# Kernel optimization log

Measured on AMD Instinct MI355X. Metric: run time of the kernel, lower is better.

## Reference

```python
import jax, jax.numpy as jnp
import numpy as np


def setup_inputs() -> dict:
    key = jax.random.key(0)
    ks = jax.random.split(key, 7)
    B, S, E = 2, 4096, 512
    return {
        "query": jax.random.normal(ks[0], (B, S, E), jnp.float32),
        "key": jax.random.normal(ks[1], (B, S, E), jnp.float32),
        "value": jax.random.normal(ks[2], (B, S, E), jnp.float32),
        "in_proj_weight": jax.random.normal(ks[3], (3 * E, E), jnp.float32) * 0.02,
        "in_proj_bias": jax.random.normal(ks[4], (3 * E,), jnp.float32) * 0.02,
        "out_proj_weight": jax.random.normal(ks[5], (E, E), jnp.float32) * 0.02,
        "out_proj_bias": jax.random.normal(ks[6], (E,), jnp.float32) * 0.02,
        "window_size": 512,
        "stride": 256,
    }


def reference(query, key, value, in_proj_weight, in_proj_bias,
              out_proj_weight, out_proj_bias, window_size, stride):
    B, S, E = query.shape
    H = 8
    hd = E // H
    scale = 1.0 / np.sqrt(hd).astype(np.float32)

    # Project full sequences once (equivalent to projecting each window slice).
    wq, wk, wv = in_proj_weight[:E], in_proj_weight[E:2 * E], in_proj_weight[2 * E:]
    bq, bk, bv = in_proj_bias[:E], in_proj_bias[E:2 * E], in_proj_bias[2 * E:]
    qp = query @ wq.T + bq   # [B,S,E]
    kp = key @ wk.T + bk
    vp = value @ wv.T + bv

    # Overlapping window gather: [nw, W] token indices.
    starts = np.arange(0, S - window_size + 1, stride)
    idx = starts[:, None] + np.arange(window_size)[None, :]  # [nw, W]
    nw, W = idx.shape

    def heads(x):  # [B,S,E] -> [B,nw,W,H,hd]
        return x[:, idx].reshape(B, nw, W, H, hd)

    qh, kh, vh = heads(qp), heads(kp), heads(vp)

    scores = jnp.einsum('bnqhd,bnkhd->bnhqk', qh, kh) * scale  # [B,nw,H,W,W]
    probs = jax.nn.softmax(scores, axis=-1)
    ctx = jnp.einsum('bnhqk,bnkhd->bnqhd', probs, vh)           # [B,nw,W,H,hd]
    ctx = ctx.reshape(B, nw * W, E)                             # concat over windows
    return ctx @ out_proj_weight.T + out_proj_bias              # [B, nw*W, E]
```

## Files before the change

kernel.cpp:

```cpp
#include <hip/hip_runtime.h>
#include <hip/hip_bf16.h>

typedef __bf16 bf16x8 __attribute__((ext_vector_type(8)));
typedef float f32x4 __attribute__((ext_vector_type(4)));
typedef float f32x16 __attribute__((ext_vector_type(16)));

__device__ __forceinline__ ushort f2bf(float f) {
  union { float f; unsigned u; } x; x.f = f;
  unsigned r = x.u + 0x7fffu + ((x.u >> 16) & 1u);
  return (ushort)(r >> 16);
}

__device__ __forceinline__ void gld_lds16(const void* g, void* l) {
  __builtin_amdgcn_global_load_lds(
      (const __attribute__((address_space(1))) void*)g,
      (__attribute__((address_space(3))) void*)l, 16, 0, 0);
}

#define VMWAIT2 asm volatile("s_waitcnt vmcnt(2)" ::: "memory")
#define VMWAIT4 asm volatile("s_waitcnt vmcnt(4)" ::: "memory")
#define VMWAIT0 asm volatile("s_waitcnt vmcnt(0)" ::: "memory")
#define LGKM0   asm volatile("s_waitcnt lgkmcnt(0)" ::: "memory")
#define SCHEDB  __builtin_amdgcn_sched_barrier(0)
#define RBAR    __builtin_amdgcn_s_barrier()

__global__ __launch_bounds__(256) void k_cvt_w(
    const float* __restrict__ wi, const float* __restrict__ wo,
    ushort* __restrict__ dst) {
  const int NWI = 196608, NWO = 65536;
  const int total = NWI + NWO;
  int i = blockIdx.x * 256 + threadIdx.x;
  int stride = gridDim.x * 256;
  for (; i < total; i += stride) {
    const float* s; int j;
    if (i < NWI) { s = wi; j = i; }
    else         { s = wo; j = i - NWI; }
    float4 val = reinterpret_cast<const float4*>(s)[j];
    ushort4 o;
    o.x = f2bf(val.x); o.y = f2bf(val.y); o.z = f2bf(val.z); o.w = f2bf(val.w);
    reinterpret_cast<ushort4*>(dst)[i] = o;
  }
}

__global__ __launch_bounds__(256) void k_gemm_qkv(
    const float* __restrict__ za0, const float* __restrict__ za1,
    const float* __restrict__ za2,
    const ushort* __restrict__ Btbase,
    const float* __restrict__ biasbase,
    ushort* __restrict__ Cbase, float qs)
{
  int bid0 = blockIdx.x;
  int bid = (bid0 & 7) * 96 + (bid0 >> 3);
  int yy = bid & 3;
  int rest = bid >> 2;
  int xx = rest & 63;
  int z = rest >> 6;

  const float* A32 = (z == 0) ? za0 : (z == 1) ? za1 : za2;
  const ushort* Bt = Btbase + (size_t)262144 * z;
  const float* bias = biasbase + 512 * z;
  float osc = (z == 0) ? qs : 1.0f;

  __shared__ ushort As[2][4096];
  __shared__ ushort Bs[3][4096];

  int tid = threadIdx.x;
  int wv = tid >> 6, ln = tid & 63;
  int l15 = ln & 15, lg = ln >> 4;
  int wm = wv >> 1, wn = wv & 1;
  int m0 = xx * 128, n0 = yy * 128;

  int row_s = tid >> 1, kh = (tid & 1) * 16;
  const float* aP = A32 + (size_t)(m0 + row_s) * 512 + kh;
  int ldsOff = row_s * 32 + kh;

#define STAGE_B(KT, BUF)                                                      \
  {                                                                           \
    _Pragma("unroll")                                                         \
    for (int h2 = 0; h2 < 2; ++h2) {                                          \
      int c = h2 * 256 + wv * 64 + ln;                                        \
      int row = c >> 2, kc = (c & 3) * 8;                                     \
      gld_lds16(Bt + (size_t)(n0 + row) * 512 + (KT) * 32 + kc,               \
                (char*)&Bs[BUF][0] + (h2 * 256 + wv * 64) * 16);              \
    }                                                                         \
  }

#define CVT_WRITE_A(F0, F1, F2, F3, BUF)                                      \
  {                                                                           \
    uint w0, w1, w2, w3, w4, w5, w6, w7;                                      \
    asm("v_cvt_pk_bf16_f32 %0, %1, %2" : "=v"(w0) : "v"(F0.x), "v"(F0.y));    \
    asm("v_cvt_pk_bf16_f32 %0, %1, %2" : "=v"(w1) : "v"(F0.z), "v"(F0.w));    \
    asm("v_cvt_pk_bf16_f32 %0, %1, %2" : "=v"(w2) : "v"(F1.x), "v"(F1.y));    \
    asm("v_cvt_pk_bf16_f32 %0, %1, %2" : "=v"(w3) : "v"(F1.z), "v"(F1.w));    \
    asm("v_cvt_pk_bf16_f32 %0, %1, %2" : "=v"(w4) : "v"(F2.x), "v"(F2.y));    \
    asm("v_cvt_pk_bf16_f32 %0, %1, %2" : "=v"(w5) : "v"(F2.z), "v"(F2.w));    \
    asm("v_cvt_pk_bf16_f32 %0, %1, %2" : "=v"(w6) : "v"(F3.x), "v"(F3.y));    \
    asm("v_cvt_pk_bf16_f32 %0, %1, %2" : "=v"(w7) : "v"(F3.z), "v"(F3.w));    \
    uint4 p0; p0.x = w0; p0.y = w1; p0.z = w2; p0.w = w3;                     \
    uint4 p1; p1.x = w4; p1.y = w5; p1.z = w6; p1.w = w7;                     \
    reinterpret_cast<uint4*>(&As[BUF][ldsOff])[0] = p0;                       \
    reinterpret_cast<uint4*>(&As[BUF][ldsOff + 8])[0] = p1;                   \
  }

  f32x4 acc[4][4] = {};

  STAGE_B(0, 0);
  float4 g0 = reinterpret_cast<const float4*>(aP)[0];
  float4 g1 = reinterpret_cast<const float4*>(aP)[1];
  float4 g2 = reinterpret_cast<const float4*>(aP)[2];
  float4 g3 = reinterpret_cast<const float4*>(aP)[3];
  STAGE_B(1, 1);
  VMWAIT2; SCHEDB;
  CVT_WRITE_A(g0, g1, g2, g3, 0);
  LGKM0; SCHEDB;
  RBAR;

#pragma unroll
  for (int kt = 0; kt < 16; ++kt) {
    const int cur = kt & 1;
    const int bcur = kt % 3;
    float4 f0, f1, f2, f3;
    if (kt < 15) {
      const float* ap = aP + (kt + 1) * 32;
      f0 = reinterpret_cast<const float4*>(ap)[0];
      f1 = reinterpret_cast<const float4*>(ap)[1];
      f2 = reinterpret_cast<const float4*>(ap)[2];
      f3 = reinterpret_cast<const float4*>(ap)[3];
    }
    if (kt < 14) STAGE_B(kt + 2, (kt + 2) % 3);

    bf16x8 af[4], bf4[4];
#pragma unroll
    for (int mf = 0; mf < 4; ++mf)
      af[mf] = *reinterpret_cast<const bf16x8*>(&As[cur][(wm * 64 + mf * 16 + l15) * 32 + lg * 8]);
#pragma unroll
    for (int nf = 0; nf < 4; ++nf)
      bf4[nf] = *reinterpret_cast<const bf16x8*>(&Bs[bcur][(wn * 64 + nf * 16 + l15) * 32 + lg * 8]);
#pragma unroll
    for (int mf = 0; mf < 4; ++mf)
#pragma unroll
      for (int nf = 0; nf < 4; ++nf)
        acc[mf][nf] = __builtin_amdgcn_mfma_f32_16x16x32_bf16(af[mf], bf4[nf], acc[mf][nf], 0, 0, 0);

    if (kt < 15) {
      if (kt < 14) { VMWAIT2; } else { VMWAIT0; }
      SCHEDB;
      CVT_WRITE_A(f0, f1, f2, f3, cur ^ 1);
      LGKM0; SCHEDB;
      RBAR;
    }
  }

#pragma unroll
  for (int mf = 0; mf < 4; ++mf)
#pragma unroll
    for (int nf = 0; nf < 4; ++nf)
#pragma unroll
      for (int r = 0; r < 4; ++r) {
        int rr = m0 + wm * 64 + mf * 16 + lg * 4 + r;
        int cc = n0 + wn * 64 + nf * 16 + l15;
        float v = (acc[mf][nf][r] + bias[cc]) * osc;
        (Cbase + (size_t)4194304 * z)[(size_t)rr * 512 + cc] = f2bf(v);
      }
#undef STAGE_B
#undef CVT_WRITE_A
}

__global__ __launch_bounds__(256) void k_gemm_out(
    const ushort* __restrict__ Ab, const ushort* __restrict__ Bt,
    const float* __restrict__ bias, float* __restrict__ C)
{
  int bid0 = blockIdx.x;
  int bid = (bid0 & 7) * 60 + (bid0 >> 3);
  int yy = bid & 3;
  int xx = bid >> 2;

  __shared__ ushort As[3][4096];
  __shared__ ushort Bs[3][4096];

  int tid = threadIdx.x;
  int wv = tid >> 6, ln = tid & 63;
  int l15 = ln & 15, lg = ln >> 4;
  int wm = wv >> 1, wn = wv & 1;
  int m0 = xx * 128, n0 = yy * 128;

#define STAGE_AB(KT, BUF)                                                     \
  {                                                                           \
    _Pragma("unroll")                                                         \
    for (int h2 = 0; h2 < 2; ++h2) {                                          \
      int c = h2 * 256 + wv * 64 + ln;                                        \
      int row = c >> 2, kc = (c & 3) * 8;                                     \
      gld_lds16(Ab + (size_t)(m0 + row) * 512 + (KT) * 32 + kc,               \
                (char*)&As[BUF][0] + (h2 * 256 + wv * 64) * 16);              \
      gld_lds16(Bt + (size_t)(n0 + row) * 512 + (KT) * 32 + kc,               \
                (char*)&Bs[BUF][0] + (h2 * 256 + wv * 64) * 16);              \
    }                                                                         \
  }

  f32x4 acc[4][4] = {};

  STAGE_AB(0, 0);
  STAGE_AB(1, 1);
  VMWAIT4; SCHEDB;
  RBAR;

#pragma unroll
  for (int kt = 0; kt < 16; ++kt) {
    const int bcur = kt % 3;
    if (kt < 14) STAGE_AB(kt + 2, (kt + 2) % 3);

    bf16x8 af[4], bf4[4];
#pragma unroll
    for (int mf = 0; mf < 4; ++mf)
      af[mf] = *reinterpret_cast<const bf16x8*>(&As[bcur][(wm * 64 + mf * 16 + l15) * 32 + lg * 8]);
#pragma unroll
    for (int nf = 0; nf < 4; ++nf)
      bf4[nf] = *reinterpret_cast<const bf16x8*>(&Bs[bcur][(wn * 64 + nf * 16 + l15) * 32 + lg * 8]);
#pragma unroll
    for (int mf = 0; mf < 4; ++mf)
#pragma unroll
      for (int nf = 0; nf < 4; ++nf)
        acc[mf][nf] = __builtin_amdgcn_mfma_f32_16x16x32_bf16(af[mf], bf4[nf], acc[mf][nf], 0, 0, 0);

    if (kt < 15) {
      if (kt < 14) { VMWAIT4; } else { VMWAIT0; }
      SCHEDB;
      RBAR;
    }
  }

#pragma unroll
  for (int mf = 0; mf < 4; ++mf)
#pragma unroll
    for (int nf = 0; nf < 4; ++nf)
#pragma unroll
      for (int r = 0; r < 4; ++r) {
        int rr = m0 + wm * 64 + mf * 16 + lg * 4 + r;
        int cc = n0 + wn * 64 + nf * 16 + l15;
        C[(size_t)rr * 512 + cc] = acc[mf][nf][r] + bias[cc];
      }
#undef STAGE_AB
}

__global__ __launch_bounds__(256, 2) void k_attn(
    const ushort* __restrict__ qp, const ushort* __restrict__ kp,
    const ushort* __restrict__ vp, ushort* __restrict__ ctx)
{
  const int E = 512, SEQ = 4096;
  int bid0 = blockIdx.x;
  int bid = (bid0 & 7) * 60 + (bid0 >> 3);
  int qh = bid & 1;
  int h = (bid >> 1) & 7;
  int n = (bid >> 4) % 15;
  int b = bid / 240;
  int start = n * 256;

  int tid = threadIdx.x;
  int w = tid >> 6, ln = tid & 63;
  int l31 = ln & 31, hi = ln >> 5;

  size_t base = ((size_t)(b * SEQ + start)) * E + h * 64;
  const ushort* Kw = kp + base;
  const ushort* Vw = vp + base;
  const ushort* Qw = qp + base;

  __shared__ ushort Vt[32768];

  {
    int sk = (tid & 63) * 8;
    int sd = (tid >> 6) * 16;
    const ushort* src = Vw + (size_t)sk * E + sd;
    union { uint4 q[2]; ushort u[16]; } R0, R1, R2, R3, R4, R5, R6, R7;
    R0.q[0] = *(const uint4*)(src + 0 * E); R0.q[1] = *(const uint4*)(src + 0 * E + 8);
    R1.q[0] = *(const uint4*)(src + 1 * E); R1.q[1] = *(const uint4*)(src + 1 * E + 8);
    R2.q[0] = *(const uint4*)(src + 2 * E); R2.q[1] = *(const uint4*)(src + 2 * E + 8);
    R3.q[0] = *(const uint4*)(src + 3 * E); R3.q[1] = *(const uint4*)(src + 3 * E + 8);
    R4.q[0] = *(const uint4*)(src + 4 * E); R4.q[1] = *(const uint4*)(src + 4 * E + 8);
    R5.q[0] = *(const uint4*)(src + 5 * E); R5.q[1] = *(const uint4*)(src + 5 * E + 8);
    R6.q[0] = *(const uint4*)(src + 6 * E); R6.q[1] = *(const uint4*)(src + 6 * E + 8);
    R7.q[0] = *(const uint4*)(src + 7 * E); R7.q[1] = *(const uint4*)(src + 7 * E + 8);
#pragma unroll
    for (int d0 = 0; d0 < 16; ++d0) {
      int d = sd + d0;
      uint4 val;
      val.x = (uint)R0.u[d0] | ((uint)R1.u[d0] << 16);
      val.y = (uint)R2.u[d0] | ((uint)R3.u[d0] << 16);
      val.z = (uint)R4.u[d0] | ((uint)R5.u[d0] << 16);
      val.w = (uint)R6.u[d0] | ((uint)R7.u[d0] << 16);
      int off = d * 1024 + ((sk * 2) ^ ((d & 7) << 4));
      *(uint4*)((char*)Vt + off) = val;
    }
  }
  __syncthreads();

  int q0 = qh * 256 + w * 64;

  bf16x8 qa0, qa1, qa2, qa3, qb0, qb1, qb2, qb3;
  {
    const ushort* qra = Qw + (size_t)(q0 + l31) * E + hi * 8;
    const ushort* qrb = qra + (size_t)32 * E;
    qa0 = *reinterpret_cast<const bf16x8*>(qra + 0);
    qa1 = *reinterpret_cast<const bf16x8*>(qra + 16);
    qa2 = *reinterpret_cast<const bf16x8*>(qra + 32);
    qa3 = *reinterpret_cast<const bf16x8*>(qra + 48);
    qb0 = *reinterpret_cast<const bf16x8*>(qrb + 0);
    qb1 = *reinterpret_cast<const bf16x8*>(qrb + 16);
    qb2 = *reinterpret_cast<const bf16x8*>(qrb + 32);
    qb3 = *reinterpret_cast<const bf16x8*>(qrb + 48);
  }

  f32x16 ca0 = {}, ca1 = {}, cb0_ = {}, cb1_ = {};
  float psa = 0.f, psb = 0.f;
  const char* lb = (const char*)Vt;

#pragma unroll
  for (int kb = 0; kb < 16; ++kb) {
    bf16x8 kf0, kf1, kf2, kf3;
    {
      const ushort* kr = Kw + (size_t)(kb * 32 + l31) * E + hi * 8;
      kf0 = *reinterpret_cast<const bf16x8*>(kr + 0);
      kf1 = *reinterpret_cast<const bf16x8*>(kr + 16);
      kf2 = *reinterpret_cast<const bf16x8*>(kr + 32);
      kf3 = *reinterpret_cast<const bf16x8*>(kr + 48);
    }
    bf16x8 vb00, vb01, vb10, vb11;
    {
      int row = l31, rowh = 32 + l31;
      int cb0 = kb * 64 + hi * 16;
      int cb1 = cb0 + 32;
      int xr0 = (row & 7) << 4;
      vb00 = *reinterpret_cast<const bf16x8*>(lb + row * 1024 + (cb0 ^ xr0));
      vb01 = *reinterpret_cast<const bf16x8*>(lb + rowh * 1024 + (cb0 ^ xr0));
      vb10 = *reinterpret_cast<const bf16x8*>(lb + row * 1024 + (cb1 ^ xr0));
      vb11 = *reinterpret_cast<const bf16x8*>(lb + rowh * 1024 + (cb1 ^ xr0));
    }

    f32x16 s1 = {}, s2 = {};
    __builtin_amdgcn_s_setprio(1);
    s1 = __builtin_amdgcn_mfma_f32_32x32x16_bf16(kf0, qa0, s1, 0, 0, 0);
    s2 = __builtin_amdgcn_mfma_f32_32x32x16_bf16(kf0, qb0, s2, 0, 0, 0);
    s1 = __builtin_amdgcn_mfma_f32_32x32x16_bf16(kf1, qa1, s1, 0, 0, 0);
    s2 = __builtin_amdgcn_mfma_f32_32x32x16_bf16(kf1, qb1, s2, 0, 0, 0);
    s1 = __builtin_amdgcn_mfma_f32_32x32x16_bf16(kf2, qa2, s1, 0, 0, 0);
    s2 = __builtin_amdgcn_mfma_f32_32x32x16_bf16(kf2, qb2, s2, 0, 0, 0);
    s1 = __builtin_amdgcn_mfma_f32_32x32x16_bf16(kf3, qa3, s1, 0, 0, 0);
    s2 = __builtin_amdgcn_mfma_f32_32x32x16_bf16(kf3, qb3, s2, 0, 0, 0);
    __builtin_amdgcn_s_setprio(0);

#pragma unroll
    for (int r = 0; r < 16; ++r) s1[r] = __builtin_amdgcn_exp2f(s1[r]);
#pragma unroll
    for (int r = 0; r < 16; ++r) s2[r] = __builtin_amdgcn_exp2f(s2[r]);
    {
      float t0 = (s1[0] + s1[1]) + (s1[2] + s1[3]);
      float t1 = (s1[4] + s1[5]) + (s1[6] + s1[7]);
      float t2 = (s1[8] + s1[9]) + (s1[10] + s1[11]);
      float t3 = (s1[12] + s1[13]) + (s1[14] + s1[15]);
      psa += (t0 + t1) + (t2 + t3);
      float u0 = (s2[0] + s2[1]) + (s2[2] + s2[3]);
      float u1 = (s2[4] + s2[5]) + (s2[6] + s2[7]);
      float u2 = (s2[8] + s2[9]) + (s2[10] + s2[11]);
      float u3 = (s2[12] + s2[13]) + (s2[14] + s2[15]);
      psb += (u0 + u1) + (u2 + u3);
    }

    uint a0, a1, a2, a3, a4, a5, a6, a7;
    asm("v_cvt_pk_bf16_f32 %0, %1, %2" : "=v"(a0) : "v"(s1[0]),  "v"(s1[1]));
    asm("v_cvt_pk_bf16_f32 %0, %1, %2" : "=v"(a1) : "v"(s1[2]),  "v"(s1[3]));
    asm("v_cvt_pk_bf16_f32 %0, %1, %2" : "=v"(a2) : "v"(s1[4]),  "v"(s1[5]));
    asm("v_cvt_pk_bf16_f32 %0, %1, %2" : "=v"(a3) : "v"(s1[6]),  "v"(s1[7]));
    asm("v_cvt_pk_bf16_f32 %0, %1, %2" : "=v"(a4) : "v"(s1[8]),  "v"(s1[9]));
    asm("v_cvt_pk_bf16_f32 %0, %1, %2" : "=v"(a5) : "v"(s1[10]), "v"(s1[11]));
    asm("v_cvt_pk_bf16_f32 %0, %1, %2" : "=v"(a6) : "v"(s1[12]), "v"(s1[13]));
    asm("v_cvt_pk_bf16_f32 %0, %1, %2" : "=v"(a7) : "v"(s1[14]), "v"(s1[15]));
    asm("v_permlane32_swap_b32 %0, %1" : "+v"(a0), "+v"(a2));
    asm("v_permlane32_swap_b32 %0, %1" : "+v"(a1), "+v"(a3));
    asm("v_permlane32_swap_b32 %0, %1" : "+v"(a4), "+v"(a6));
    asm("v_permlane32_swap_b32 %0, %1" : "+v"(a5), "+v"(a7));
    uint b0, b1, b2, b3, b4, b5, b6, b7;
    asm("v_cvt_pk_bf16_f32 %0, %1, %2" : "=v"(b0) : "v"(s2[0]),  "v"(s2[1]));
    asm("v_cvt_pk_bf16_f32 %0, %1, %2" : "=v"(b1) : "v"(s2[2]),  "v"(s2[3]));
    asm("v_cvt_pk_bf16_f32 %0, %1, %2" : "=v"(b2) : "v"(s2[4]),  "v"(s2[5]));
    asm("v_cvt_pk_bf16_f32 %0, %1, %2" : "=v"(b3) : "v"(s2[6]),  "v"(s2[7]));
    asm("v_cvt_pk_bf16_f32 %0, %1, %2" : "=v"(b4) : "v"(s2[8]),  "v"(s2[9]));
    asm("v_cvt_pk_bf16_f32 %0, %1, %2" : "=v"(b5) : "v"(s2[10]), "v"(s2[11]));
    asm("v_cvt_pk_bf16_f32 %0, %1, %2" : "=v"(b6) : "v"(s2[12]), "v"(s2[13]));
    asm("v_cvt_pk_bf16_f32 %0, %1, %2" : "=v"(b7) : "v"(s2[14]), "v"(s2[15]));
    asm("v_permlane32_swap_b32 %0, %1" : "+v"(b0), "+v"(b2));
    asm("v_permlane32_swap_b32 %0, %1" : "+v"(b1), "+v"(b3));
    asm("v_permlane32_swap_b32 %0, %1" : "+v"(b4), "+v"(b6));
    asm("v_permlane32_swap_b32 %0, %1" : "+v"(b5), "+v"(b7));
    union { uint u[4]; bf16x8 v; } A1, A2, B1, B2;
    A1.u[0] = a0; A1.u[1] = a1; A1.u[2] = a2; A1.u[3] = a3;
    A2.u[0] = a4; A2.u[1] = a5; A2.u[2] = a6; A2.u[3] = a7;
    B1.u[0] = b0; B1.u[1] = b1; B1.u[2] = b2; B1.u[3] = b3;
    B2.u[0] = b4; B2.u[1] = b5; B2.u[2] = b6; B2.u[3] = b7;

    __builtin_amdgcn_s_setprio(1);
    ca0  = __builtin_amdgcn_mfma_f32_32x32x16_bf16(A1.v, vb00, ca0, 0, 0, 0);
    cb0_ = __builtin_amdgcn_mfma_f32_32x32x16_bf16(B1.v, vb00, cb0_, 0, 0, 0);
    ca1  = __builtin_amdgcn_mfma_f32_32x32x16_bf16(A1.v, vb01, ca1, 0, 0, 0);
    cb1_ = __builtin_amdgcn_mfma_f32_32x32x16_bf16(B1.v, vb01, cb1_, 0, 0, 0);
    ca0  = __builtin_amdgcn_mfma_f32_32x32x16_bf16(A2.v, vb10, ca0, 0, 0, 0);
    cb0_ = __builtin_amdgcn_mfma_f32_32x32x16_bf16(B2.v, vb10, cb0_, 0, 0, 0);
    ca1  = __builtin_amdgcn_mfma_f32_32x32x16_bf16(A2.v, vb11, ca1, 0, 0, 0);
    cb1_ = __builtin_amdgcn_mfma_f32_32x32x16_bf16(B2.v, vb11, cb1_, 0, 0, 0);
    __builtin_amdgcn_s_setprio(0);
  }

  psa += __shfl_xor(psa, 32);
  psb += __shfl_xor(psb, 32);
  float ria = 1.0f / psa;
  float rib = 1.0f / psb;
  size_t orow0 = (size_t)b * 7680 + (size_t)n * 512 + q0;
#pragma unroll
  for (int r = 0; r < 16; ++r) {
    int qrel = (r & 3) + 8 * (r >> 2) + 4 * hi;
    float r1 = __shfl(ria, qrel);
    float r2 = __shfl(rib, qrel);
    ushort* dA = ctx + (orow0 + qrel) * E + h * 64 + l31;
    ushort* dB = ctx + (orow0 + 32 + qrel) * E + h * 64 + l31;
    dA[0]  = f2bf(ca0[r] * r1);
    dA[32] = f2bf(ca1[r] * r1);
    dB[0]  = f2bf(cb0_[r] * r2);
    dB[32] = f2bf(cb1_[r] * r2);
  }
}

extern "C" void kernel_launch(void* const* d_in, const int* in_sizes, int n_in,
                              void* d_out, int out_size, void* d_ws, size_t ws_size,
                              hipStream_t stream) {
  const float* query = (const float*)d_in[0];
  const float* key   = (const float*)d_in[1];
  const float* value = (const float*)d_in[2];
  const float* ipw   = (const float*)d_in[3];
  const float* ipb   = (const float*)d_in[4];
  const float* opw   = (const float*)d_in[5];
  const float* opb   = (const float*)d_in[6];

  ushort* wib = (ushort*)d_ws;
  ushort* wob = wib + 786432;
  ushort* qp  = wob + 262144;
  ushort* kp  = qp  + 4194304;
  ushort* vp  = kp  + 4194304;
  ushort* ctx = vp  + 4194304;

  const float SC = 0.125f * 1.44269504088896340736f;

  k_cvt_w<<<512, 256, 0, stream>>>(ipw, opw, wib);

  k_gemm_qkv<<<768, 256, 0, stream>>>(
      query, key, value, wib, ipb, qp, SC);

  k_attn<<<480, 256, 0, stream>>>(qp, kp, vp, ctx);

  k_gemm_out<<<480, 256, 0, stream>>>(
      ctx, wob, opb, (float*)d_out);
}
```

Before: 81.72 us.

## Pre-convert Q/K/V activations to bf16 and use async LDS loads in QKV GEMM

Extends the weight conversion kernel so it also converts the query, key and value inputs to bf16 in a workspace buffer. The QKV projection GEMM then reads bf16 A operands through direct global-to-LDS loads with triple buffering, like the output GEMM. The old in-kernel fp32 load, convert and LDS write path is removed. This simplifies the GEMM main loop, but adds a full extra pass that reads the fp32 activations and writes bf16 copies to memory.

```diff
diff --git a/kernel.cpp b/kernel.cpp
--- a/kernel.cpp
+++ b/kernel.cpp
@@ -17,24 +17,27 @@
       (__attribute__((address_space(3))) void*)l, 16, 0, 0);
 }
 
-#define VMWAIT2 asm volatile("s_waitcnt vmcnt(2)" ::: "memory")
-#define VMWAIT4 asm volatile("s_waitcnt vmcnt(4)" ::: "memory")
-#define VMWAIT0 asm volatile("s_waitcnt vmcnt(0)" ::: "memory")
-#define LGKM0   asm volatile("s_waitcnt lgkmcnt(0)" ::: "memory")
-#define SCHEDB  __builtin_amdgcn_sched_barrier(0)
-#define RBAR    __builtin_amdgcn_s_barrier()
-
-__global__ __launch_bounds__(256) void k_cvt_w(
-    const float* __restrict__ wi, const float* __restrict__ wo,
-    ushort* __restrict__ dst) {
+#define VMW4   asm volatile("s_waitcnt vmcnt(4)" ::: "memory")
+#define VMW0   asm volatile("s_waitcnt vmcnt(0)" ::: "memory")
+#define SCHEDB __builtin_amdgcn_sched_barrier(0)
+#define RBAR   __builtin_amdgcn_s_barrier()
+
+__global__ __launch_bounds__(256) void k_cvt_all(
+    const float* __restrict__ q, const float* __restrict__ k,
+    const float* __restrict__ v, const float* __restrict__ wi,
+    const float* __restrict__ wo, ushort* __restrict__ dst) {
+  const int NQ = 1048576;
   const int NWI = 196608, NWO = 65536;
-  const int total = NWI + NWO;
+  const int total = 3 * NQ + NWI + NWO;
   int i = blockIdx.x * 256 + threadIdx.x;
   int stride = gridDim.x * 256;
   for (; i < total; i += stride) {
     const float* s; int j;
-    if (i < NWI) { s = wi; j = i; }
-    else         { s = wo; j = i - NWI; }
+    if (i < NQ)              { s = q;  j = i; }
+    else if (i < 2 * NQ)     { s = k;  j = i - NQ; }
+    else if (i < 3 * NQ)     { s = v;  j = i - 2 * NQ; }
+    else if (i < 3 * NQ + NWI) { s = wi; j = i - 3 * NQ; }
+    else                     { s = wo; j = i - 3 * NQ - NWI; }
     float4 val = reinterpret_cast<const float4*>(s)[j];
     ushort4 o;
     o.x = f2bf(val.x); o.y = f2bf(val.y); o.z = f2bf(val.z); o.w = f2bf(val.w);
@@ -43,8 +46,7 @@
 }
 
 __global__ __launch_bounds__(256) void k_gemm_qkv(
-    const float* __restrict__ za0, const float* __restrict__ za1,
-    const float* __restrict__ za2,
+    const ushort* __restrict__ Abase,
     const ushort* __restrict__ Btbase,
     const float* __restrict__ biasbase,
     ushort* __restrict__ Cbase, float qs)
@@ -56,124 +58,10 @@
   int xx = rest & 63;
   int z = rest >> 6;
 
-  const float* A32 = (z == 0) ? za0 : (z == 1) ? za1 : za2;
+  const ushort* Ab = Abase + (size_t)4194304 * z;
   const ushort* Bt = Btbase + (size_t)262144 * z;
   const float* bias = biasbase + 512 * z;
   float osc = (z == 0) ? qs : 1.0f;
-
-  __shared__ ushort As[2][4096];
-  __shared__ ushort Bs[3][4096];
-
-  int tid = threadIdx.x;
-  int wv = tid >> 6, ln = tid & 63;
-  int l15 = ln & 15, lg = ln >> 4;
-  int wm = wv >> 1, wn = wv & 1;
-  int m0 = xx * 128, n0 = yy * 128;
-
-  int row_s = tid >> 1, kh = (tid & 1) * 16;
-  const float* aP = A32 + (size_t)(m0 + row_s) * 512 + kh;
-  int ldsOff = row_s * 32 + kh;
-
-#define STAGE_B(KT, BUF)                                                      \
-  {                                                                           \
-    _Pragma("unroll")                                                         \
-    for (int h2 = 0; h2 < 2; ++h2) {                                          \
-      int c = h2 * 256 + wv * 64 + ln;                                        \
-      int row = c >> 2, kc = (c & 3) * 8;                                     \
-      gld_lds16(Bt + (size_t)(n0 + row) * 512 + (KT) * 32 + kc,               \
-                (char*)&Bs[BUF][0] + (h2 * 256 + wv * 64) * 16);              \
-    }                                                                         \
-  }
-
-#define CVT_WRITE_A(F0, F1, F2, F3, BUF)                                      \
-  {                                                                           \
-    uint w0, w1, w2, w3, w4, w5, w6, w7;                                      \
-    asm("v_cvt_pk_bf16_f32 %0, %1, %2" : "=v"(w0) : "v"(F0.x), "v"(F0.y));    \
-    asm("v_cvt_pk_bf16_f32 %0, %1, %2" : "=v"(w1) : "v"(F0.z), "v"(F0.w));    \
-    asm("v_cvt_pk_bf16_f32 %0, %1, %2" : "=v"(w2) : "v"(F1.x), "v"(F1.y));    \
-    asm("v_cvt_pk_bf16_f32 %0, %1, %2" : "=v"(w3) : "v"(F1.z), "v"(F1.w));    \
-    asm("v_cvt_pk_bf16_f32 %0, %1, %2" : "=v"(w4) : "v"(F2.x), "v"(F2.y));    \
-    asm("v_cvt_pk_bf16_f32 %0, %1, %2" : "=v"(w5) : "v"(F2.z), "v"(F2.w));    \
-    asm("v_cvt_pk_bf16_f32 %0, %1, %2" : "=v"(w6) : "v"(F3.x), "v"(F3.y));    \
-    asm("v_cvt_pk_bf16_f32 %0, %1, %2" : "=v"(w7) : "v"(F3.z), "v"(F3.w));    \
-    uint4 p0; p0.x = w0; p0.y = w1; p0.z = w2; p0.w = w3;                     \
-    uint4 p1; p1.x = w4; p1.y = w5; p1.z = w6; p1.w = w7;                     \
-    reinterpret_cast<uint4*>(&As[BUF][ldsOff])[0] = p0;                       \
-    reinterpret_cast<uint4*>(&As[BUF][ldsOff + 8])[0] = p1;                   \
-  }
-
-  f32x4 acc[4][4] = {};
-
-  STAGE_B(0, 0);
-  float4 g0 = reinterpret_cast<const float4*>(aP)[0];
-  float4 g1 = reinterpret_cast<const float4*>(aP)[1];
-  float4 g2 = reinterpret_cast<const float4*>(aP)[2];
-  float4 g3 = reinterpret_cast<const float4*>(aP)[3];
-  STAGE_B(1, 1);
-  VMWAIT2; SCHEDB;
-  CVT_WRITE_A(g0, g1, g2, g3, 0);
-  LGKM0; SCHEDB;
-  RBAR;
-
-#pragma unroll
-  for (int kt = 0; kt < 16; ++kt) {
-    const int cur = kt & 1;
-    const int bcur = kt % 3;
-    float4 f0, f1, f2, f3;
-    if (kt < 15) {
-      const float* ap = aP + (kt + 1) * 32;
-      f0 = reinterpret_cast<const float4*>(ap)[0];
-      f1 = reinterpret_cast<const float4*>(ap)[1];
-      f2 = reinterpret_cast<const float4*>(ap)[2];
-      f3 = reinterpret_cast<const float4*>(ap)[3];
-    }
-    if (kt < 14) STAGE_B(kt + 2, (kt + 2) % 3);
-
-    bf16x8 af[4], bf4[4];
-#pragma unroll
-    for (int mf = 0; mf < 4; ++mf)
-      af[mf] = *reinterpret_cast<const bf16x8*>(&As[cur][(wm * 64 + mf * 16 + l15) * 32 + lg * 8]);
-#pragma unroll
-    for (int nf = 0; nf < 4; ++nf)
-      bf4[nf] = *reinterpret_cast<const bf16x8*>(&Bs[bcur][(wn * 64 + nf * 16 + l15) * 32 + lg * 8]);
-#pragma unroll
-    for (int mf = 0; mf < 4; ++mf)
-#pragma unroll
-      for (int nf = 0; nf < 4; ++nf)
-        acc[mf][nf] = __builtin_amdgcn_mfma_f32_16x16x32_bf16(af[mf], bf4[nf], acc[mf][nf], 0, 0, 0);
-
-    if (kt < 15) {
-      if (kt < 14) { VMWAIT2; } else { VMWAIT0; }
-      SCHEDB;
-      CVT_WRITE_A(f0, f1, f2, f3, cur ^ 1);
-      LGKM0; SCHEDB;
-      RBAR;
-    }
-  }
-
-#pragma unroll
-  for (int mf = 0; mf < 4; ++mf)
-#pragma unroll
-    for (int nf = 0; nf < 4; ++nf)
-#pragma unroll
-      for (int r = 0; r < 4; ++r) {
-        int rr = m0 + wm * 64 + mf * 16 + lg * 4 + r;
-        int cc = n0 + wn * 64 + nf * 16 + l15;
-        float v = (acc[mf][nf][r] + bias[cc]) * osc;
-        (Cbase + (size_t)4194304 * z)[(size_t)rr * 512 + cc] = f2bf(v);
-      }
-#undef STAGE_B
-#undef CVT_WRITE_A
-}
-
-__global__ __launch_bounds__(256) void k_gemm_out(
-    const ushort* __restrict__ Ab, const ushort* __restrict__ Bt,
-    const float* __restrict__ bias, float* __restrict__ C)
-{
-  int bid0 = blockIdx.x;
-  int bid = (bid0 & 7) * 60 + (bid0 >> 3);
-  int yy = bid & 3;
-  int xx = bid >> 2;
 
   __shared__ ushort As[3][4096];
   __shared__ ushort Bs[3][4096];
@@ -201,7 +89,7 @@
 
   STAGE_AB(0, 0);
   STAGE_AB(1, 1);
-  VMWAIT4; SCHEDB;
+  VMW4; SCHEDB;
   RBAR;
 
 #pragma unroll
@@ -223,7 +111,84 @@
         acc[mf][nf] = __builtin_amdgcn_mfma_f32_16x16x32_bf16(af[mf], bf4[nf], acc[mf][nf], 0, 0, 0);
 
     if (kt < 15) {
-      if (kt < 14) { VMWAIT4; } else { VMWAIT0; }
+      if (kt < 14) { VMW4; } else { VMW0; }
+      SCHEDB;
+      RBAR;
+    }
+  }
+
+#pragma unroll
+  for (int mf = 0; mf < 4; ++mf)
+#pragma unroll
+    for (int nf = 0; nf < 4; ++nf)
+#pragma unroll
+      for (int r = 0; r < 4; ++r) {
+        int rr = m0 + wm * 64 + mf * 16 + lg * 4 + r;
+        int cc = n0 + wn * 64 + nf * 16 + l15;
+        float v = (acc[mf][nf][r] + bias[cc]) * osc;
+        (Cbase + (size_t)4194304 * z)[(size_t)rr * 512 + cc] = f2bf(v);
+      }
+#undef STAGE_AB
+}
+
+__global__ __launch_bounds__(256) void k_gemm_out(
+    const ushort* __restrict__ Ab, const ushort* __restrict__ Bt,
+    const float* __restrict__ bias, float* __restrict__ C)
+{
+  int bid0 = blockIdx.x;
+  int bid = (bid0 & 7) * 60 + (bid0 >> 3);
+  int yy = bid & 3;
+  int xx = bid >> 2;
+
+  __shared__ ushort As[3][4096];
+  __shared__ ushort Bs[3][4096];
+
+  int tid = threadIdx.x;
+  int wv = tid >> 6, ln = tid & 63;
+  int l15 = ln & 15, lg = ln >> 4;
+  int wm = wv >> 1, wn = wv & 1;
+  int m0 = xx * 128, n0 = yy * 128;
+
+#define STAGE_AB(KT, BUF)                                                     \
+  {                                                                           \
+    _Pragma("unroll")                                                         \
+    for (int h2 = 0; h2 < 2; ++h2) {                                          \
+      int c = h2 * 256 + wv * 64 + ln;                                        \
+      int row = c >> 2, kc = (c & 3) * 8;                                     \
+      gld_lds16(Ab + (size_t)(m0 + row) * 512 + (KT) * 32 + kc,               \
+                (char*)&As[BUF][0] + (h2 * 256 + wv * 64) * 16);              \
+      gld_lds16(Bt + (size_t)(n0 + row) * 512 + (KT) * 32 + kc,               \
+                (char*)&Bs[BUF][0] + (h2 * 256 + wv * 64) * 16);              \
+    }                                                                         \
+  }
+
+  f32x4 acc[4][4] = {};
+
+  STAGE_AB(0, 0);
+  STAGE_AB(1, 1);
+  VMW4; SCHEDB;
+  RBAR;
+
+#pragma unroll
+  for (int kt = 0; kt < 16; ++kt) {
+    const int bcur = kt % 3;
+    if (kt < 14) STAGE_AB(kt + 2, (kt + 2) % 3);
+
+    bf16x8 af[4], bf4[4];
+#pragma unroll
+    for (int mf = 0; mf < 4; ++mf)
+      af[mf] = *reinterpret_cast<const bf16x8*>(&As[bcur][(wm * 64 + mf * 16 + l15) * 32 + lg * 8]);
+#pragma unroll
+    for (int nf = 0; nf < 4; ++nf)
+      bf4[nf] = *reinterpret_cast<const bf16x8*>(&Bs[bcur][(wn * 64 + nf * 16 + l15) * 32 + lg * 8]);
+#pragma unroll
+    for (int mf = 0; mf < 4; ++mf)
+#pragma unroll
+      for (int nf = 0; nf < 4; ++nf)
+        acc[mf][nf] = __builtin_amdgcn_mfma_f32_16x16x32_bf16(af[mf], bf4[nf], acc[mf][nf], 0, 0, 0);
+
+    if (kt < 15) {
+      if (kt < 14) { VMW4; } else { VMW0; }
       SCHEDB;
       RBAR;
     }
@@ -438,7 +403,10 @@
   const float* opw   = (const float*)d_in[5];
   const float* opb   = (const float*)d_in[6];
 
-  ushort* wib = (ushort*)d_ws;
+  ushort* qb  = (ushort*)d_ws;
+  ushort* kb  = qb  + 4194304;
+  ushort* vb  = kb  + 4194304;
+  ushort* wib = vb  + 4194304;
   ushort* wob = wib + 786432;
   ushort* qp  = wob + 262144;
   ushort* kp  = qp  + 4194304;
@@ -447,13 +415,11 @@
 
   const float SC = 0.125f * 1.44269504088896340736f;
 
-  k_cvt_w<<<512, 256, 0, stream>>>(ipw, opw, wib);
-
-  k_gemm_qkv<<<768, 256, 0, stream>>>(
-      query, key, value, wib, ipb, qp, SC);
+  k_cvt_all<<<2048, 256, 0, stream>>>(query, key, value, ipw, opw, qb);
+
+  k_gemm_qkv<<<768, 256, 0, stream>>>(qb, wib, ipb, qp, SC);
 
   k_attn<<<480, 256, 0, stream>>>(qp, kp, vp, ctx);
 
-  k_gemm_out<<<480, 256, 0, stream>>>(
-      ctx, wob, opb, (float*)d_out);
-}
+  k_gemm_out<<<480, 256, 0, stream>>>(ctx, wob, opb, (float*)d_out);
+}
```

Measured after the change: 84.08 us. +2.9%, slower.

## Split attention blocks over head-dim halves to double grid and occupancy

Applied to the files above, without the earlier changes.

Each attention block now handles only half of the 64-wide head dimension for the PV product, which doubles the grid from 480 to 960 blocks. This halves the V-transpose LDS buffer and the output accumulators, and raises the launch-bounds occupancy hint from 2 to 3. The cost is that QK^T scores and softmax are now computed twice per query tile, once for each half. Several macros are renamed with no behavioural change.

```diff
diff --git a/kernel.cpp b/kernel.cpp
--- a/kernel.cpp
+++ b/kernel.cpp
@@ -17,12 +17,12 @@
       (__attribute__((address_space(3))) void*)l, 16, 0, 0);
 }
 
-#define VMWAIT2 asm volatile("s_waitcnt vmcnt(2)" ::: "memory")
-#define VMWAIT4 asm volatile("s_waitcnt vmcnt(4)" ::: "memory")
-#define VMWAIT0 asm volatile("s_waitcnt vmcnt(0)" ::: "memory")
-#define LGKM0   asm volatile("s_waitcnt lgkmcnt(0)" ::: "memory")
-#define SCHEDB  __builtin_amdgcn_sched_barrier(0)
-#define RBAR    __builtin_amdgcn_s_barrier()
+#define VMW2   asm volatile("s_waitcnt vmcnt(2)" ::: "memory")
+#define VMW4   asm volatile("s_waitcnt vmcnt(4)" ::: "memory")
+#define VMW0   asm volatile("s_waitcnt vmcnt(0)" ::: "memory")
+#define LGKM0  asm volatile("s_waitcnt lgkmcnt(0)" ::: "memory")
+#define SCHEDB __builtin_amdgcn_sched_barrier(0)
+#define RBAR   __builtin_amdgcn_s_barrier()
 
 __global__ __launch_bounds__(256) void k_cvt_w(
     const float* __restrict__ wi, const float* __restrict__ wo,
@@ -110,7 +110,7 @@
   float4 g2 = reinterpret_cast<const float4*>(aP)[2];
   float4 g3 = reinterpret_cast<const float4*>(aP)[3];
   STAGE_B(1, 1);
-  VMWAIT2; SCHEDB;
+  VMW2; SCHEDB;
   CVT_WRITE_A(g0, g1, g2, g3, 0);
   LGKM0; SCHEDB;
   RBAR;
@@ -143,7 +143,7 @@
         acc[mf][nf] = __builtin_amdgcn_mfma_f32_16x16x32_bf16(af[mf], bf4[nf], acc[mf][nf], 0, 0, 0);
 
     if (kt < 15) {
-      if (kt < 14) { VMWAIT2; } else { VMWAIT0; }
+      if (kt < 14) { VMW2; } else { VMW0; }
       SCHEDB;
       CVT_WRITE_A(f0, f1, f2, f3, cur ^ 1);
       LGKM0; SCHEDB;
@@ -201,7 +201,7 @@
 
   STAGE_AB(0, 0);
   STAGE_AB(1, 1);
-  VMWAIT4; SCHEDB;
+  VMW4; SCHEDB;
   RBAR;
 
 #pragma unroll
@@ -223,7 +223,7 @@
         acc[mf][nf] = __builtin_amdgcn_mfma_f32_16x16x32_bf16(af[mf], bf4[nf], acc[mf][nf], 0, 0, 0);
 
     if (kt < 15) {
-      if (kt < 14) { VMWAIT4; } else { VMWAIT0; }
+      if (kt < 14) { VMW4; } else { VMW0; }
       SCHEDB;
       RBAR;
     }
@@ -242,17 +242,18 @@
 #undef STAGE_AB
 }
 
-__global__ __launch_bounds__(256, 2) void k_attn(
+__global__ __launch_bounds__(256, 3) void k_attn(
     const ushort* __restrict__ qp, const ushort* __restrict__ kp,
     const ushort* __restrict__ vp, ushort* __restrict__ ctx)
 {
   const int E = 512, SEQ = 4096;
   int bid0 = blockIdx.x;
-  int bid = (bid0 & 7) * 60 + (bid0 >> 3);
-  int qh = bid & 1;
-  int h = (bid >> 1) & 7;
-  int n = (bid >> 4) % 15;
-  int b = bid / 240;
+  int bid = (bid0 & 7) * 120 + (bid0 >> 3);
+  int dh = bid & 1;
+  int qh = (bid >> 1) & 1;
+  int h = (bid >> 2) & 7;
+  int n = (bid >> 5) % 15;
+  int b = bid / 480;
   int start = n * 256;
 
   int tid = threadIdx.x;
@@ -264,23 +265,23 @@
   const ushort* Vw = vp + base;
   const ushort* Qw = qp + base;
 
-  __shared__ ushort Vt[32768];
+  __shared__ ushort Vt[16384];
 
   {
     int sk = (tid & 63) * 8;
-    int sd = (tid >> 6) * 16;
-    const ushort* src = Vw + (size_t)sk * E + sd;
-    union { uint4 q[2]; ushort u[16]; } R0, R1, R2, R3, R4, R5, R6, R7;
-    R0.q[0] = *(const uint4*)(src + 0 * E); R0.q[1] = *(const uint4*)(src + 0 * E + 8);
-    R1.q[0] = *(const uint4*)(src + 1 * E); R1.q[1] = *(const uint4*)(src + 1 * E + 8);
-    R2.q[0] = *(const uint4*)(src + 2 * E); R2.q[1] = *(const uint4*)(src + 2 * E + 8);
-    R3.q[0] = *(const uint4*)(src + 3 * E); R3.q[1] = *(const uint4*)(src + 3 * E + 8);
-    R4.q[0] = *(const uint4*)(src + 4 * E); R4.q[1] = *(const uint4*)(src + 4 * E + 8);
-    R5.q[0] = *(const uint4*)(src + 5 * E); R5.q[1] = *(const uint4*)(src + 5 * E + 8);
-    R6.q[0] = *(const uint4*)(src + 6 * E); R6.q[1] = *(const uint4*)(src + 6 * E + 8);
-    R7.q[0] = *(const uint4*)(src + 7 * E); R7.q[1] = *(const uint4*)(src + 7 * E + 8);
-#pragma unroll
-    for (int d0 = 0; d0 < 16; ++d0) {
+    int sd = (tid >> 6) * 8;
+    const ushort* src = Vw + (size_t)sk * E + dh * 32 + sd;
+    union { uint4 q; ushort u[8]; } R0, R1, R2, R3, R4, R5, R6, R7;
+    R0.q = *(const uint4*)(src + 0 * E);
+    R1.q = *(const uint4*)(src + 1 * E);
+    R2.q = *(const uint4*)(src + 2 * E);
+    R3.q = *(const uint4*)(src + 3 * E);
+    R4.q = *(const uint4*)(src + 4 * E);
+    R5.q = *(const uint4*)(src + 5 * E);
+    R6.q = *(const uint4*)(src + 6 * E);
+    R7.q = *(const uint4*)(src + 7 * E);
+#pragma unroll
+    for (int d0 = 0; d0 < 8; ++d0) {
       int d = sd + d0;
       uint4 val;
       val.x = (uint)R0.u[d0] | ((uint)R1.u[d0] << 16);
@@ -309,7 +310,7 @@
     qb3 = *reinterpret_cast<const bf16x8*>(qrb + 48);
   }
 
-  f32x16 ca0 = {}, ca1 = {}, cb0_ = {}, cb1_ = {};
+  f32x16 ca = {}, cb = {};
   float psa = 0.f, psb = 0.f;
   const char* lb = (const char*)Vt;
 
@@ -323,16 +324,13 @@
       kf2 = *reinterpret_cast<const bf16x8*>(kr + 32);
       kf3 = *reinterpret_cast<const bf16x8*>(kr + 48);
     }
-    bf16x8 vb00, vb01, vb10, vb11;
+    bf16x8 vb0, vb1;
     {
-      int row = l31, rowh = 32 + l31;
       int cb0 = kb * 64 + hi * 16;
       int cb1 = cb0 + 32;
-      int xr0 = (row & 7) << 4;
-      vb00 = *reinterpret_cast<const bf16x8*>(lb + row * 1024 + (cb0 ^ xr0));
-      vb01 = *reinterpret_cast<const bf16x8*>(lb + rowh * 1024 + (cb0 ^ xr0));
-      vb10 = *reinterpret_cast<const bf16x8*>(lb + row * 1024 + (cb1 ^ xr0));
-      vb11 = *reinterpret_cast<const bf16x8*>(lb + rowh * 1024 + (cb1 ^ xr0));
+      int xr0 = (l31 & 7) << 4;
+      vb0 = *reinterpret_cast<const bf16x8*>(lb + l31 * 1024 + (cb0 ^ xr0));
+      vb1 = *reinterpret_cast<const bf16x8*>(lb + l31 * 1024 + (cb1 ^ xr0));
     }
 
     f32x16 s1 = {}, s2 = {};
@@ -397,14 +395,10 @@
     B2.u[0] = b4; B2.u[1] = b5; B2.u[2] = b6; B2.u[3] = b7;
 
     __builtin_amdgcn_s_setprio(1);
-    ca0  = __builtin_amdgcn_mfma_f32_32x32x16_bf16(A1.v, vb00, ca0, 0, 0, 0);
-    cb0_ = __builtin_amdgcn_mfma_f32_32x32x16_bf16(B1.v, vb00, cb0_, 0, 0, 0);
-    ca1  = __builtin_amdgcn_mfma_f32_32x32x16_bf16(A1.v, vb01, ca1, 0, 0, 0);
-    cb1_ = __builtin_amdgcn_mfma_f32_32x32x16_bf16(B1.v, vb01, cb1_, 0, 0, 0);
-    ca0  = __builtin_amdgcn_mfma_f32_32x32x16_bf16(A2.v, vb10, ca0, 0, 0, 0);
-    cb0_ = __builtin_amdgcn_mfma_f32_32x32x16_bf16(B2.v, vb10, cb0_, 0, 0, 0);
-    ca1  = __builtin_amdgcn_mfma_f32_32x32x16_bf16(A2.v, vb11, ca1, 0, 0, 0);
-    cb1_ = __builtin_amdgcn_mfma_f32_32x32x16_bf16(B2.v, vb11, cb1_, 0, 0, 0);
+    ca = __builtin_amdgcn_mfma_f32_32x32x16_bf16(A1.v, vb0, ca, 0, 0, 0);
+    cb = __builtin_amdgcn_mfma_f32_32x32x16_bf16(B1.v, vb0, cb, 0, 0, 0);
+    ca = __builtin_amdgcn_mfma_f32_32x32x16_bf16(A2.v, vb1, ca, 0, 0, 0);
+    cb = __builtin_amdgcn_mfma_f32_32x32x16_bf16(B2.v, vb1, cb, 0, 0, 0);
     __builtin_amdgcn_s_setprio(0);
   }
 
@@ -418,12 +412,8 @@
     int qrel = (r & 3) + 8 * (r >> 2) + 4 * hi;
     float r1 = __shfl(ria, qrel);
     float r2 = __shfl(rib, qrel);
-    ushort* dA = ctx + (orow0 + qrel) * E + h * 64 + l31;
-    ushort* dB = ctx + (orow0 + 32 + qrel) * E + h * 64 + l31;
-    dA[0]  = f2bf(ca0[r] * r1);
-    dA[32] = f2bf(ca1[r] * r1);
-    dB[0]  = f2bf(cb0_[r] * r2);
-    dB[32] = f2bf(cb1_[r] * r2);
+    ctx[(orow0 + qrel) * E + h * 64 + dh * 32 + l31]      = f2bf(ca[r] * r1);
+    ctx[(orow0 + 32 + qrel) * E + h * 64 + dh * 32 + l31] = f2bf(cb[r] * r2);
   }
 }
 
@@ -452,7 +442,7 @@
   k_gemm_qkv<<<768, 256, 0, stream>>>(
       query, key, value, wib, ipb, qp, SC);
 
-  k_attn<<<480, 256, 0, stream>>>(qp, kp, vp, ctx);
+  k_attn<<<960, 256, 0, stream>>>(qp, kp, vp, ctx);
 
   k_gemm_out<<<480, 256, 0, stream>>>(
       ctx, wob, opb, (float*)d_out);
```

New measurement: 96.19 us. +17.7%, slower.

## Stage K tiles through triple-buffered LDS with async global-to-LDS loads in attention

Applied to the files above, without the earlier changes.

The attention kernel used to read each K block straight from global memory into registers inside the loop, which left it exposed to load latency. K tiles now go into a three-slot LDS ring buffer through global_load_lds, prefetched two blocks ahead. Reads use an XOR swizzle to avoid bank conflicts, and vmcnt waits plus a workgroup barrier follow each iteration. This hides K load latency but adds a barrier per iteration and 12KB more LDS, which may lower occupancy.

```diff
diff --git a/kernel.cpp b/kernel.cpp
--- a/kernel.cpp
+++ b/kernel.cpp
@@ -17,12 +17,13 @@
       (__attribute__((address_space(3))) void*)l, 16, 0, 0);
 }
 
-#define VMWAIT2 asm volatile("s_waitcnt vmcnt(2)" ::: "memory")
-#define VMWAIT4 asm volatile("s_waitcnt vmcnt(4)" ::: "memory")
-#define VMWAIT0 asm volatile("s_waitcnt vmcnt(0)" ::: "memory")
-#define LGKM0   asm volatile("s_waitcnt lgkmcnt(0)" ::: "memory")
-#define SCHEDB  __builtin_amdgcn_sched_barrier(0)
-#define RBAR    __builtin_amdgcn_s_barrier()
+#define VMW1   asm volatile("s_waitcnt vmcnt(1)" ::: "memory")
+#define VMW2   asm volatile("s_waitcnt vmcnt(2)" ::: "memory")
+#define VMW4   asm volatile("s_waitcnt vmcnt(4)" ::: "memory")
+#define VMW0   asm volatile("s_waitcnt vmcnt(0)" ::: "memory")
+#define LGKM0  asm volatile("s_waitcnt lgkmcnt(0)" ::: "memory")
+#define SCHEDB __builtin_amdgcn_sched_barrier(0)
+#define RBAR   __builtin_amdgcn_s_barrier()
 
 __global__ __launch_bounds__(256) void k_cvt_w(
     const float* __restrict__ wi, const float* __restrict__ wo,
@@ -110,7 +111,7 @@
   float4 g2 = reinterpret_cast<const float4*>(aP)[2];
   float4 g3 = reinterpret_cast<const float4*>(aP)[3];
   STAGE_B(1, 1);
-  VMWAIT2; SCHEDB;
+  VMW2; SCHEDB;
   CVT_WRITE_A(g0, g1, g2, g3, 0);
   LGKM0; SCHEDB;
   RBAR;
@@ -143,7 +144,7 @@
         acc[mf][nf] = __builtin_amdgcn_mfma_f32_16x16x32_bf16(af[mf], bf4[nf], acc[mf][nf], 0, 0, 0);
 
     if (kt < 15) {
-      if (kt < 14) { VMWAIT2; } else { VMWAIT0; }
+      if (kt < 14) { VMW2; } else { VMW0; }
       SCHEDB;
       CVT_WRITE_A(f0, f1, f2, f3, cur ^ 1);
       LGKM0; SCHEDB;
@@ -201,7 +202,7 @@
 
   STAGE_AB(0, 0);
   STAGE_AB(1, 1);
-  VMWAIT4; SCHEDB;
+  VMW4; SCHEDB;
   RBAR;
 
 #pragma unroll
@@ -223,7 +224,7 @@
         acc[mf][nf] = __builtin_amdgcn_mfma_f32_16x16x32_bf16(af[mf], bf4[nf], acc[mf][nf], 0, 0, 0);
 
     if (kt < 15) {
-      if (kt < 14) { VMWAIT4; } else { VMWAIT0; }
+      if (kt < 14) { VMW4; } else { VMW0; }
       SCHEDB;
       RBAR;
     }
@@ -265,6 +266,7 @@
   const ushort* Qw = qp + base;
 
   __shared__ ushort Vt[32768];
+  __shared__ ushort Ks[3][2048];
 
   {
     int sk = (tid & 63) * 8;
@@ -309,30 +311,47 @@
     qb3 = *reinterpret_cast<const bf16x8*>(qrb + 48);
   }
 
+#define STAGE_K(KB, BUF)                                                      \
+  {                                                                           \
+    int row_ = tid >> 3;                                                      \
+    int cs_ = (tid & 7) * 16;                                                 \
+    int del_ = (cs_ ^ ((row_ & 7) << 4)) >> 1;                                \
+    gld_lds16(Kw + (size_t)((KB) * 32 + row_) * E + del_,                     \
+              (char*)&Ks[BUF][0] + tid * 16);                                 \
+  }
+
   f32x16 ca0 = {}, ca1 = {}, cb0_ = {}, cb1_ = {};
   float psa = 0.f, psb = 0.f;
   const char* lb = (const char*)Vt;
 
+  STAGE_K(0, 0);
+  STAGE_K(1, 1);
+  VMW1; SCHEDB;
+  RBAR;
+
 #pragma unroll
   for (int kb = 0; kb < 16; ++kb) {
+    if (kb < 14) STAGE_K(kb + 2, (kb + 2) % 3);
+
     bf16x8 kf0, kf1, kf2, kf3;
     {
-      const ushort* kr = Kw + (size_t)(kb * 32 + l31) * E + hi * 8;
-      kf0 = *reinterpret_cast<const bf16x8*>(kr + 0);
-      kf1 = *reinterpret_cast<const bf16x8*>(kr + 16);
-      kf2 = *reinterpret_cast<const bf16x8*>(kr + 32);
-      kf3 = *reinterpret_cast<const bf16x8*>(kr + 48);
-    }
-    bf16x8 vb00, vb01, vb10, vb11;
+      const char* kbase = (const char*)&Ks[kb % 3][0] + l31 * 128;
+      int xr = (l31 & 7) << 4;
+      kf0 = *reinterpret_cast<const bf16x8*>(kbase + ((0 * 32 + hi * 16) ^ xr));
+      kf1 = *reinterpret_cast<const bf16x8*>(kbase + ((1 * 32 + hi * 16) ^ xr));
+      kf2 = *reinterpret_cast<const bf16x8*>(kbase + ((2 * 32 + hi * 16) ^ xr));
+      kf3 = *reinterpret_cast<const bf16x8*>(kbase + ((3 * 32 + hi * 16) ^ xr));
+    }
+    bf16x8 vb0, vb1, vb2, vb3;
     {
       int row = l31, rowh = 32 + l31;
       int cb0 = kb * 64 + hi * 16;
       int cb1 = cb0 + 32;
       int xr0 = (row & 7) << 4;
-      vb00 = *reinterpret_cast<const bf16x8*>(lb + row * 1024 + (cb0 ^ xr0));
-      vb01 = *reinterpret_cast<const bf16x8*>(lb + rowh * 1024 + (cb0 ^ xr0));
-      vb10 = *reinterpret_cast<const bf16x8*>(lb + row * 1024 + (cb1 ^ xr0));
-      vb11 = *reinterpret_cast<const bf16x8*>(lb + rowh * 1024 + (cb1 ^ xr0));
+      vb0 = *reinterpret_cast<const bf16x8*>(lb + row * 1024 + (cb0 ^ xr0));
+      vb1 = *reinterpret_cast<const bf16x8*>(lb + rowh * 1024 + (cb0 ^ xr0));
+      vb2 = *reinterpret_cast<const bf16x8*>(lb + row * 1024 + (cb1 ^ xr0));
+      vb3 = *reinterpret_cast<const bf16x8*>(lb + rowh * 1024 + (cb1 ^ xr0));
     }
 
     f32x16 s1 = {}, s2 = {};
@@ -397,16 +416,23 @@
     B2.u[0] = b4; B2.u[1] = b5; B2.u[2] = b6; B2.u[3] = b7;
 
     __builtin_amdgcn_s_setprio(1);
-    ca0  = __builtin_amdgcn_mfma_f32_32x32x16_bf16(A1.v, vb00, ca0, 0, 0, 0);
-    cb0_ = __builtin_amdgcn_mfma_f32_32x32x16_bf16(B1.v, vb00, cb0_, 0, 0, 0);
-    ca1  = __builtin_amdgcn_mfma_f32_32x32x16_bf16(A1.v, vb01, ca1, 0, 0, 0);
-    cb1_ = __builtin_amdgcn_mfma_f32_32x32x16_bf16(B1.v, vb01, cb1_, 0, 0, 0);
-    ca0  = __builtin_amdgcn_mfma_f32_32x32x16_bf16(A2.v, vb10, ca0, 0, 0, 0);
-    cb0_ = __builtin_amdgcn_mfma_f32_32x32x16_bf16(B2.v, vb10, cb0_, 0, 0, 0);
-    ca1  = __builtin_amdgcn_mfma_f32_32x32x16_bf16(A2.v, vb11, ca1, 0, 0, 0);
-    cb1_ = __builtin_amdgcn_mfma_f32_32x32x16_bf16(B2.v, vb11, cb1_, 0, 0, 0);
+    ca0  = __builtin_amdgcn_mfma_f32_32x32x16_bf16(A1.v, vb0, ca0, 0, 0, 0);
+    cb0_ = __builtin_amdgcn_mfma_f32_32x32x16_bf16(B1.v, vb0, cb0_, 0, 0, 0);
+    ca1  = __builtin_amdgcn_mfma_f32_32x32x16_bf16(A1.v, vb1, ca1, 0, 0, 0);
+    cb1_ = __builtin_amdgcn_mfma_f32_32x32x16_bf16(B1.v, vb1, cb1_, 0, 0, 0);
+    ca0  = __builtin_amdgcn_mfma_f32_32x32x16_bf16(A2.v, vb2, ca0, 0, 0, 0);
+    cb0_ = __builtin_amdgcn_mfma_f32_32x32x16_bf16(B2.v, vb2, cb0_, 0, 0, 0);
+    ca1  = __builtin_amdgcn_mfma_f32_32x32x16_bf16(A2.v, vb3, ca1, 0, 0, 0);
+    cb1_ = __builtin_amdgcn_mfma_f32_32x32x16_bf16(B2.v, vb3, cb1_, 0, 0, 0);
     __builtin_amdgcn_s_setprio(0);
-  }
+
+    if (kb < 15) {
+      if (kb < 14) { VMW1; } else { VMW0; }
+      SCHEDB;
+      RBAR;
+    }
+  }
+#undef STAGE_K
 
   psa += __shfl_xor(psa, 32);
   psb += __shfl_xor(psb, 32);
```

Measured after the change: 193.5 us. +136.8%, slower.
